# Kernel optimization log

Measured on AMD Instinct MI355X. Metric: run time of the kernel, lower is better.

The kernel has to match this reference:

```python
import jax, jax.numpy as jnp
import numpy as np
import math

# Fixed module hyperparameters (init_kwargs)
LENGTH_SCALE = 0.59
TIME_SCALE = 3.9

# Connection constants for the z -> 1/z transformation of 2F1(1/3, 17/6, 4/3, z):
#   A = G(c)G(b-a)/(G(b)G(c-a)),  B = G(c)G(a-b)/(G(a)G(c-b))
# with a=1/3, b=17/6, c=4/3 (math.gamma handles negative non-integer args).
A_COEF = math.gamma(4.0 / 3.0) * math.gamma(5.0 / 2.0) / (math.gamma(17.0 / 6.0) * math.gamma(1.0))
B_COEF = math.gamma(4.0 / 3.0) * math.gamma(-5.0 / 2.0) / (math.gamma(1.0 / 3.0) * math.gamma(-3.0 / 2.0))
# Branch split point: |t/(1+t)| == |1/t| at t = golden ratio, so both series
# arguments stay <= 0.618 and converge geometrically.
PHI = (1.0 + math.sqrt(5.0)) / 2.0
N_TERMS = 150


def _hyp_series(a, b, c, z, n_terms=N_TERMS):
    """Gauss hypergeometric series sum_n (a)_n (b)_n / ((c)_n n!) z^n, |z| < 1."""
    def body(n, carry):
        s, term = carry
        nf = jnp.asarray(n, z.dtype)
        term = term * ((a + nf) * (b + nf) / ((c + nf) * (nf + 1.0))) * z
        return (s + term, term)

    s, _ = jax.lax.fori_loop(0, n_terms, body, (jnp.ones_like(z), jnp.ones_like(z)))
    return s


def _hyp2f1_fixed(t):
    """2F1(1/3, 17/6, 4/3, -t) for t > 0, matching scipy.special.hyp2f1."""
    # Branch A (t <= PHI): Pfaff transform -> (1+t)^(-a) 2F1(a, c-b, c, t/(1+t))
    t_a = jnp.minimum(t, PHI)
    w = t_a / (1.0 + t_a)  # in [0, 0.618]
    f_a = (1.0 + t_a) ** (-1.0 / 3.0) * _hyp_series(1.0 / 3.0, -3.0 / 2.0, 4.0 / 3.0, w)

    # Branch B (t > PHI): z -> 1/z transform; the first series has parameter
    # a-c+1 = 0 so it collapses to 1.
    t_b = jnp.maximum(t, PHI)
    u = -1.0 / t_b  # in (-0.618, 0)
    f_b = (A_COEF * t_b ** (-1.0 / 3.0)
           + B_COEF * t_b ** (-17.0 / 6.0) * _hyp_series(17.0 / 6.0, 5.0 / 2.0, 7.0 / 2.0, u))

    return jnp.where(t <= PHI, f_a, f_b)


def setup_inputs() -> dict:
    key = jax.random.key(0)
    k = jax.random.normal(key, (256, 256, 256, 3), dtype=jnp.float32)
    return {"k": k}


def reference(k) -> jnp.ndarray:
    # tau(k) = time_scale * (L|k|)^(-2/3) / sqrt( 2F1(1/3, 17/6, 4/3, -(L|k|)^-2) )
    kL = LENGTH_SCALE * jnp.linalg.norm(k, axis=-1)  # [256,256,256]
    t = kL ** (-2.0)
    tau = kL ** (-2.0 / 3.0) / jnp.sqrt(_hyp2f1_fixed(t))
    return TIME_SCALE * tau
```

## Files before the change

kernel.cpp:

```cpp
#include <hip/hip_runtime.h>
#include <math.h>


#define NT 12

__host__ __device__ constexpr float coefA(int n) {
    return (float)(((1.0/3.0 + n) * (n - 1.5)) / ((4.0/3.0 + n) * (n + 1.0)));
}
__host__ __device__ constexpr float coefB(int n) {
    return (float)(((17.0/6.0 + n) * (n + 2.5)) / ((3.5 + n) * (n + 1.0)));
}

__device__ __forceinline__ float frcp(float x)   { return __builtin_amdgcn_rcpf(x); }
__device__ __forceinline__ float frsq(float x)   { return __builtin_amdgcn_rsqf(x); }
__device__ __forceinline__ float fsqrt_(float x) { return __builtin_amdgcn_sqrtf(x); }
#if __has_builtin(__builtin_amdgcn_logf)
__device__ __forceinline__ float flog2(float x)  { return __builtin_amdgcn_logf(x); }
#else
__device__ __forceinline__ float flog2(float x)  { return __log2f(x); }
#endif
#if __has_builtin(__builtin_amdgcn_exp2f)
__device__ __forceinline__ float fexp2(float x)  { return __builtin_amdgcn_exp2f(x); }
#else
__device__ __forceinline__ float fexp2(float x)  { return exp2f(x); }
#endif

__global__ __launch_bounds__(256) void mann_elt_kernel(
        const float* __restrict__ k, float* __restrict__ out, int n_elems) {
    __shared__ float s[3072];

    const int t     = threadIdx.x;
    const int chunk = blockIdx.x;
    const int ebase = chunk << 10;
    const int f4base = chunk * 768;
    const int n_f4  = (3 * n_elems) >> 2;

    const float4* __restrict__ k4 = (const float4*)k;
    #pragma unroll
    for (int i = 0; i < 3; ++i) {
        int idx4 = f4base + (i << 8) + t;
        float4 v = make_float4(0.f, 0.f, 0.f, 0.f);
        if (idx4 < n_f4) v = k4[idx4];
        float4 w = make_float4(v.x * v.x, v.y * v.y, v.z * v.z, v.w * v.w);
        ((float4*)s)[(i << 8) + t] = w;
    }
    __syncthreads();

    const float LS2 = 0.3481f;
    float q[4], z[4], acc[4], rr[4];
    bool brA[4];
    #pragma unroll
    for (int e = 0; e < 4; ++e) {
        int le = t + (e << 8);
        float s0 = s[3 * le + 0];
        float s1 = s[3 * le + 1];
        float s2 = s[3 * le + 2];
        q[e]   = LS2 * ((s0 + s1) + s2);
        brA[e] = q[e] >= 0.6180339887f;
        rr[e]  = frcp(1.0f + q[e]);
        z[e]   = brA[e] ? rr[e] : -q[e];
        acc[e] = 1.0f;
    }

    #pragma unroll
    for (int n = NT - 1; n >= 0; --n) {
        const float cA = coefA(n);
        const float cB = coefB(n);
        #pragma unroll
        for (int e = 0; e < 4; ++e) {
            float c = brA[e] ? cA : cB;
            acc[e] = fmaf(c * z[e], acc[e], 1.0f);
        }
    }

    #pragma unroll
    for (int e = 0; e < 4; ++e) {
        float qq = q[e];
        float S  = acc[e];
        float cr   = fexp2(flog2(rr[e]) * (1.0f / 3.0f));
        float argA = qq * cr * S;
        float q72  = qq * qq * qq * fsqrt_(qq);
        float argB = fmaf((-2.0f / 15.0f) * q72, S, 0.68834394f * qq);
        float arg  = brA[e] ? argA : argB;
        int ge = ebase + t + (e << 8);
        if (ge < n_elems) out[ge] = 3.9f * frsq(arg);
    }
}

extern "C" void kernel_launch(void* const* d_in, const int* in_sizes, int n_in,
                              void* d_out, int out_size, void* d_ws, size_t ws_size,
                              hipStream_t stream) {
    const float* k = (const float*)d_in[0];
    float* out = (float*)d_out;
    int n_elems = out_size;
    int blocks = (n_elems + 1023) >> 10;
    mann_elt_kernel<<<blocks, 256, 0, stream>>>(k, out, n_elems);
}
```

Measured before the change: 289.3 us.

## Drop LDS staging; each thread loads three float4s and stores one float4 non-temporally

Each thread now reads three consecutive float4s directly from global memory, which covers four complete 3-vectors, instead of staging squared inputs through shared memory behind a barrier. The four results are written as one contiguous vector using a non-temporal store. This removes the LDS traffic and the __syncthreads, at the cost of strided, less coalesced global loads of 48 bytes per thread. The tail handling now assumes the element count is divisible by 4.

After: 289.0 us. Within noise of the previous version (-0.1%).

```diff
diff --git a/kernel.cpp b/kernel.cpp
--- a/kernel.cpp
+++ b/kernel.cpp
@@ -3,6 +3,8 @@
 
 
 #define NT 12
+
+typedef float nfloat4 __attribute__((ext_vector_type(4)));
 
 __host__ __device__ constexpr float coefA(int n) {
     return (float)(((1.0/3.0 + n) * (n - 1.5)) / ((4.0/3.0 + n) * (n + 1.0)));
@@ -26,39 +28,29 @@
 #endif
 
 __global__ __launch_bounds__(256) void mann_elt_kernel(
-        const float* __restrict__ k, float* __restrict__ out, int n_elems) {
-    __shared__ float s[3072];
-
-    const int t     = threadIdx.x;
-    const int chunk = blockIdx.x;
-    const int ebase = chunk << 10;
-    const int f4base = chunk * 768;
-    const int n_f4  = (3 * n_elems) >> 2;
+        const float* __restrict__ k, float* __restrict__ out, int n_quads) {
+    int tid = blockIdx.x * blockDim.x + threadIdx.x;
+    if (tid >= n_quads) return;
 
     const float4* __restrict__ k4 = (const float4*)k;
-    #pragma unroll
-    for (int i = 0; i < 3; ++i) {
-        int idx4 = f4base + (i << 8) + t;
-        float4 v = make_float4(0.f, 0.f, 0.f, 0.f);
-        if (idx4 < n_f4) v = k4[idx4];
-        float4 w = make_float4(v.x * v.x, v.y * v.y, v.z * v.z, v.w * v.w);
-        ((float4*)s)[(i << 8) + t] = w;
-    }
-    __syncthreads();
+    float4 v0 = k4[3*tid+0];
+    float4 v1 = k4[3*tid+1];
+    float4 v2 = k4[3*tid+2];
 
     const float LS2 = 0.3481f;
-    float q[4], z[4], acc[4], rr[4];
+    float q[4];
+    q[0] = LS2 * (v0.x*v0.x + v0.y*v0.y + v0.z*v0.z);
+    q[1] = LS2 * (v0.w*v0.w + v1.x*v1.x + v1.y*v1.y);
+    q[2] = LS2 * (v1.z*v1.z + v1.w*v1.w + v2.x*v2.x);
+    q[3] = LS2 * (v2.y*v2.y + v2.z*v2.z + v2.w*v2.w);
+
     bool brA[4];
+    float z[4], acc[4], rr[4];
     #pragma unroll
     for (int e = 0; e < 4; ++e) {
-        int le = t + (e << 8);
-        float s0 = s[3 * le + 0];
-        float s1 = s[3 * le + 1];
-        float s2 = s[3 * le + 2];
-        q[e]   = LS2 * ((s0 + s1) + s2);
         brA[e] = q[e] >= 0.6180339887f;
-        rr[e]  = frcp(1.0f + q[e]);
-        z[e]   = brA[e] ? rr[e] : -q[e];
+        rr[e] = frcp(1.0f + q[e]);
+        z[e] = brA[e] ? rr[e] : -q[e];
         acc[e] = 1.0f;
     }
 
@@ -73,18 +65,22 @@
         }
     }
 
+    float res[4];
     #pragma unroll
     for (int e = 0; e < 4; ++e) {
         float qq = q[e];
         float S  = acc[e];
-        float cr   = fexp2(flog2(rr[e]) * (1.0f / 3.0f));
+        float cr   = fexp2(flog2(rr[e]) * (1.0f/3.0f));
         float argA = qq * cr * S;
         float q72  = qq * qq * qq * fsqrt_(qq);
-        float argB = fmaf((-2.0f / 15.0f) * q72, S, 0.68834394f * qq);
+        float argB = fmaf((-2.0f/15.0f) * q72, S, 0.68834394f * qq);
         float arg  = brA[e] ? argA : argB;
-        int ge = ebase + t + (e << 8);
-        if (ge < n_elems) out[ge] = 3.9f * frsq(arg);
+        res[e] = 3.9f * frsq(arg);
     }
+
+    nfloat4 r;
+    r.x = res[0]; r.y = res[1]; r.z = res[2]; r.w = res[3];
+    __builtin_nontemporal_store(r, (nfloat4*)out + tid);
 }
 
 extern "C" void kernel_launch(void* const* d_in, const int* in_sizes, int n_in,
@@ -92,7 +88,8 @@
                               hipStream_t stream) {
     const float* k = (const float*)d_in[0];
     float* out = (float*)d_out;
-    int n_elems = out_size;
-    int blocks = (n_elems + 1023) >> 10;
-    mann_elt_kernel<<<blocks, 256, 0, stream>>>(k, out, n_elems);
+    int n_quads = out_size / 4;
+    int threads = 256;
+    int blocks = (n_quads + threads - 1) / threads;
+    mann_elt_kernel<<<blocks, threads, 0, stream>>>(k, out, n_quads);
 }
```
